# Optimization experiments

Hardware: AMD Instinct MI355X
Metric: run time of the kernel (lower is better)

The kernel has to match this reference:

```python
import jax, jax.numpy as jnp
import numpy as np

N_NODES = 100000


def gcn_conv(x, src, dst, W, b, n_nodes):
    """PyG GCNConv: out = D^{-1/2} (A + I) D^{-1/2} (x @ W) + b.
    src/dst are the original (non-self-loop) edges; self loops handled analytically.
    """
    h = x @ W  # [N, out]
    ones = jnp.ones(src.shape[0], dtype=h.dtype)
    # degree including self loop
    deg = jax.ops.segment_sum(ones, dst, num_segments=n_nodes) + 1.0  # [N]
    dinv = jax.lax.rsqrt(deg)
    norm = dinv[src] * dinv[dst]  # [E]
    msg = h[src] * norm[:, None]  # gather + scale
    agg = jax.ops.segment_sum(msg, dst, num_segments=n_nodes)  # scatter-add
    # self-loop contribution: norm = deg^{-1/2} * deg^{-1/2} = 1/deg
    agg = agg + h * (1.0 / deg)[:, None]
    return agg + b


def setup_inputs() -> dict:
    key = jax.random.key(0)
    k1, k2, k3, k4 = jax.random.split(key, 4)
    n, e = N_NODES, 3200000
    x = jax.random.normal(k1, (n, 256), dtype=jnp.float32)
    edge_index = jax.random.randint(k2, (2, e), 0, n, dtype=jnp.int64)
    W1 = jax.random.normal(k3, (256, 64), dtype=jnp.float32) * (1.0 / np.sqrt(256))
    b1 = jnp.zeros((64,), dtype=jnp.float32)
    W2 = jax.random.normal(k4, (64, 4), dtype=jnp.float32) * (1.0 / np.sqrt(64))
    b2 = jnp.zeros((4,), dtype=jnp.float32)
    return {"x": x, "edge_index": edge_index, "W1": W1, "b1": b1, "W2": W2, "b2": b2}


def reference(x, edge_index, W1, b1, W2, b2):
    n = x.shape[0]
    src, dst = edge_index[0], edge_index[1]
    h = gcn_conv(x, src, dst, W1, b1, n)
    h = jax.nn.leaky_relu(h, negative_slope=0.01)  # nn.LeakyReLU default
    # F.dropout in eval mode is identity
    h = gcn_conv(h, src, dst, W2, b2, n)
    return jax.nn.softmax(h, axis=1)
```

## Files before the change

### kernel.cpp

```cpp
#include <hip/hip_runtime.h>
#include <hip/hip_bf16.h>
#include <math.h>


#define NB 256
#define MAXB 512
#define SCHUNK 12544

typedef __attribute__((ext_vector_type(8))) short bf16x8;
typedef __attribute__((ext_vector_type(4))) float f32x4;
typedef __attribute__((ext_vector_type(2))) float f32x2;
typedef __attribute__((ext_vector_type(4))) float nf4;

__device__ __forceinline__ int edge_val(const void* ep, size_t idx, int is64) {
    if (is64) return (int)(((const long long*)ep)[idx]);
    return ((const int*)ep)[idx];
}

__device__ __forceinline__ int detect64(const unsigned int* __restrict__ ew, int E) {
    const int lane = (int)(threadIdx.x & 63);
    const int idx = (lane < E) ? (2 * lane + 1) : 1;
    const unsigned long long m = __ballot(ew[idx] != 0u);
    return m == 0ull ? 1 : 0;
}

__device__ __forceinline__ unsigned short f2bf(float f) {
    unsigned int u = __float_as_uint(f);
    return (unsigned short)((u + 0x7FFFu + ((u >> 16) & 1u)) >> 16);
}

__device__ __forceinline__ void acc_fp8row(unsigned int r, float& a0, float& a1,
                                           float& a2, float& a3) {
    const f32x2 lo = __builtin_amdgcn_cvt_pk_f32_fp8((int)r, false);
    const f32x2 hi = __builtin_amdgcn_cvt_pk_f32_fp8((int)r, true);
    a0 += lo[0]; a1 += lo[1]; a2 += hi[0]; a3 += hi[1];
}

__device__ __forceinline__ unsigned char f32_to_fp8(float f) {
    const int enc = __builtin_amdgcn_cvt_pk_fp8_f32(f, 0.f, 0, false);
    return (unsigned char)(enc & 0xff);
}

__global__ __launch_bounds__(256) void hist_pass(
    const void* __restrict__ edges, int E, int* __restrict__ ghist, int B) {
    __shared__ int hist[MAXB];
    const int tid = threadIdx.x;
    for (int i = tid; i < B; i += 256) hist[i] = 0;
    const int is64 = detect64((const unsigned int*)edges, E);
    __syncthreads();
    const int per = (E + NB - 1) / NB;
    const int s0 = blockIdx.x * per;
    const int s1 = min(s0 + per, E);
    for (int i = s0 + tid; i < s1; i += 256) {
        const int d = edge_val(edges, (size_t)E + i, is64);
        atomicAdd(&hist[d >> 8], 1);
    }
    __syncthreads();
    for (int i = tid; i < B; i += 256) ghist[(size_t)blockIdx.x * B + i] = hist[i];
}

__global__ __launch_bounds__(NB) void col_scan(
    const int* __restrict__ ghist, int* __restrict__ goff,
    int* __restrict__ bsum, int B) {
    __shared__ int sm[NB];
    const int tid = threadIdx.x;
    const int b = blockIdx.x;
    const int v = ghist[(size_t)tid * B + b];
    sm[tid] = v;
    __syncthreads();
    for (int off = 1; off < NB; off <<= 1) {
        int val = (tid >= off) ? sm[tid - off] : 0;
        __syncthreads();
        sm[tid] += val;
        __syncthreads();
    }
    goff[(size_t)tid * B + b] = sm[tid] - v;
    if (tid == NB - 1) bsum[b] = sm[tid];
}

__global__ __launch_bounds__(512) void base_scan(
    const int* __restrict__ bsum, int* __restrict__ bbase,
    int* __restrict__ row_ptr, int B, int n, int E) {
    __shared__ int sm[512];
    const int tid = threadIdx.x;
    const int v = (tid < B) ? bsum[tid] : 0;
    sm[tid] = v;
    __syncthreads();
    for (int off = 1; off < 512; off <<= 1) {
        int val = (tid >= off) ? sm[tid - off] : 0;
        __syncthreads();
        sm[tid] += val;
        __syncthreads();
    }
    if (tid < B) bbase[tid] = sm[tid] - v;
    if (tid == 0) { bbase[B] = E; row_ptr[n] = E; }
}

__global__ __launch_bounds__(512) void scatter_pass(
    const void* __restrict__ edges, int E,
    const int* __restrict__ ghist, const int* __restrict__ goff,
    const int* __restrict__ bbase, unsigned int* __restrict__ ebuf, int B) {
    __shared__ unsigned int buf[SCHUNK];
    __shared__ int lb[MAXB];
    __shared__ int lf[MAXB];
    __shared__ int sm[MAXB];
    const int tid = threadIdx.x;
    const int blk = blockIdx.x;
    const int is64 = detect64((const unsigned int*)edges, E);
    const int per = (E + NB - 1) / NB;
    const int s0 = blk * per;
    const int s1 = min(s0 + per, E);

    if (per <= SCHUNK) {
        const int c = (tid < B) ? ghist[(size_t)blk * B + tid] : 0;
        sm[tid] = c;
        __syncthreads();
        for (int off = 1; off < MAXB; off <<= 1) {
            int val = (tid >= off) ? sm[tid - off] : 0;
            __syncthreads();
            sm[tid] += val;
            __syncthreads();
        }
        if (tid < B) { lb[tid] = sm[tid] - c; lf[tid] = sm[tid] - c; }
        __syncthreads();
        for (int i = s0 + tid; i < s1; i += 512) {
            const int d = edge_val(edges, (size_t)E + i, is64);
            const int s = edge_val(edges, (size_t)i, is64);
            const unsigned int val = ((unsigned int)s << 8) | (unsigned int)(d & 255);
            const int pos = atomicAdd(&lf[d >> 8], 1);
            buf[pos] = val;
        }
        __syncthreads();
        const int lane = tid & 63;
        const int wv = tid >> 6;
        for (int b = wv; b < B; b += 8) {
            const int lo = lb[b];
            const int cnt = lf[b] - lo;
            if (cnt > 0) {
                unsigned int* dst = ebuf + bbase[b] + goff[(size_t)blk * B + b];
                for (int k = lane; k < cnt; k += 64) dst[k] = buf[lo + k];
            }
        }
    } else {
        for (int i = tid; i < B; i += 512)
            lf[i] = bbase[i] + goff[(size_t)blk * B + i];
        __syncthreads();
        for (int i = s0 + tid; i < s1; i += 512) {
            const int d = edge_val(edges, (size_t)E + i, is64);
            const int s = edge_val(edges, (size_t)i, is64);
            const int pos = atomicAdd(&lf[d >> 8], 1);
            ebuf[pos] = ((unsigned int)s << 8) | (unsigned int)(d & 255);
        }
    }
}

__global__ __launch_bounds__(512) void bucket_csr(
    const unsigned int* __restrict__ ebuf, const int* __restrict__ bbase,
    int* __restrict__ row_ptr, float* __restrict__ dinv,
    int* __restrict__ col_src, int n) {
    __shared__ int hist[256];
    __shared__ int scn[256];
    __shared__ int fill[256];
    const int tid = threadIdx.x;
    const int b = blockIdx.x;
    if (tid < 256) hist[tid] = 0;
    __syncthreads();
    const int base = bbase[b];
    const int m = bbase[b + 1] - base;
    const unsigned int* eb = ebuf + base;
    for (int i = tid; i < m; i += 512) atomicAdd(&hist[eb[i] & 255u], 1);
    __syncthreads();
    if (tid < 256) scn[tid] = hist[tid];
    __syncthreads();
    for (int off = 1; off < 256; off <<= 1) {
        int val = 0;
        if (tid < 256 && tid >= off) val = scn[tid - off];
        __syncthreads();
        if (tid < 256) scn[tid] += val;
        __syncthreads();
    }
    if (tid < 256) {
        const int excl = scn[tid] - hist[tid];
        fill[tid] = excl;
        const int v = b * 256 + tid;
        if (v < n) {
            row_ptr[v] = base + excl;
            dinv[v] = rsqrtf((float)hist[tid] + 1.0f);
        }
    }
    __syncthreads();
    for (int i = tid; i < m; i += 512) {
        const unsigned int e = eb[i];
        const int p = atomicAdd(&fill[e & 255u], 1);
        col_src[base + p] = (int)(e >> 8);
    }
}

__global__ __launch_bounds__(256) void gemm1_kernel(
    const float* __restrict__ x, const float* __restrict__ W1,
    const float* __restrict__ dinv, unsigned char* __restrict__ hs1f8, int n) {
    __shared__ unsigned short wt[64 * 264];
    const int tid = threadIdx.x;
    for (int i = tid; i < 4096; i += 256) {
        const int k = i >> 4;
        const int c0 = (i & 15) * 4;
        const float4 w = *((const float4*)W1 + i);
        wt[(c0 + 0) * 264 + k] = f2bf(w.x);
        wt[(c0 + 1) * 264 + k] = f2bf(w.y);
        wt[(c0 + 2) * 264 + k] = f2bf(w.z);
        wt[(c0 + 3) * 264 + k] = f2bf(w.w);
    }
    __syncthreads();

    const int lane = tid & 63;
    const int wid = tid >> 6;
    const int row0 = blockIdx.x * 64 + wid * 16;
    const int rr = lane & 15;
    const int kh = lane >> 4;

    union FragU { bf16x8 v; unsigned short u[8]; };
    bf16x8 af[8];
    {
        int r = row0 + rr;
        if (r >= n) r = n - 1;
        const float* xr = x + (size_t)r * 256 + kh * 8;
#pragma unroll
        for (int ks = 0; ks < 8; ++ks) {
            const nf4 p0 = __builtin_nontemporal_load((const nf4*)(xr + ks * 32));
            const nf4 p1 = __builtin_nontemporal_load((const nf4*)(xr + ks * 32 + 4));
            FragU f;
            f.u[0] = f2bf(p0[0]); f.u[1] = f2bf(p0[1]);
            f.u[2] = f2bf(p0[2]); f.u[3] = f2bf(p0[3]);
            f.u[4] = f2bf(p1[0]); f.u[5] = f2bf(p1[1]);
            f.u[6] = f2bf(p1[2]); f.u[7] = f2bf(p1[3]);
            af[ks] = f.v;
        }
    }
    f32x4 acc[4];
#pragma unroll
    for (int ct = 0; ct < 4; ++ct) acc[ct] = (f32x4){0.f, 0.f, 0.f, 0.f};
#pragma unroll
    for (int ct = 0; ct < 4; ++ct) {
        const unsigned short* wcol = wt + (ct * 16 + rr) * 264 + kh * 8;
#pragma unroll
        for (int ks = 0; ks < 8; ++ks) {
            const bf16x8 bf = *(const bf16x8*)(wcol + ks * 32);
            acc[ct] = __builtin_amdgcn_mfma_f32_16x16x32_bf16(af[ks], bf, acc[ct], 0, 0, 0);
        }
    }
#pragma unroll
    for (int j = 0; j < 4; ++j) {
        const int gr = row0 + kh * 4 + j;
        if (gr < n) {
            const float dv = dinv[gr];
#pragma unroll
            for (int ct = 0; ct < 4; ++ct)
                hs1f8[(size_t)gr * 64 + ct * 16 + rr] = f32_to_fp8(acc[ct][j] * dv);
        }
    }
}

__global__ __launch_bounds__(256) void agg1_kernel(
    const int* __restrict__ row_ptr, const int* __restrict__ col_src,
    const unsigned char* __restrict__ hs1f8, const float* __restrict__ dinv,
    const float* __restrict__ b1, const float* __restrict__ W2,
    float* __restrict__ hs2, int n) {
    const int tid = threadIdx.x;
    const int q = tid & 15;
    const int v = blockIdx.x * 16 + (tid >> 4);
    if (v >= n) return;
    const int rs = row_ptr[v];
    const int re = row_ptr[v + 1];
    float a0 = 0.f, a1 = 0.f, a2 = 0.f, a3 = 0.f;
    int e = rs;
    for (; e + 16 <= re; e += 16) {
        const int cs = col_src[e + q];
        unsigned int r[16];
#pragma unroll
        for (int j = 0; j < 16; ++j) {
            const int s = __shfl(cs, j, 16);
            r[j] = *(const unsigned int*)(hs1f8 + (size_t)s * 64 + q * 4);
        }
#pragma unroll
        for (int j = 0; j < 16; ++j) acc_fp8row(r[j], a0, a1, a2, a3);
    }
    const int rem = re - e;
    if (rem > 0) {
        const int cs = col_src[(q < rem) ? e + q : re - 1];
        for (int j = 0; j < rem; ++j) {
            const int s = __shfl(cs, j, 16);
            const unsigned int r = *(const unsigned int*)(hs1f8 + (size_t)s * 64 + q * 4);
            acc_fp8row(r, a0, a1, a2, a3);
        }
    }
    float s0 = 0.f, s1 = 0.f, s2 = 0.f, s3 = 0.f;
    acc_fp8row(*(const unsigned int*)(hs1f8 + (size_t)v * 64 + q * 4), s0, s1, s2, s3);
    const float dv = dinv[v];
    const float4 bb = ((const float4*)b1)[q];
    float4 res;
    res.x = dv * (a0 + s0) + bb.x;
    res.y = dv * (a1 + s1) + bb.y;
    res.z = dv * (a2 + s2) + bb.z;
    res.w = dv * (a3 + s3) + bb.w;
    res.x = res.x > 0.f ? res.x : 0.01f * res.x;
    res.y = res.y > 0.f ? res.y : 0.01f * res.y;
    res.z = res.z > 0.f ? res.z : 0.01f * res.z;
    res.w = res.w > 0.f ? res.w : 0.01f * res.w;
    const float4* W2v = (const float4*)W2;
    const float4 w0 = W2v[q * 4 + 0], w1 = W2v[q * 4 + 1];
    const float4 w2 = W2v[q * 4 + 2], w3 = W2v[q * 4 + 3];
    float4 p;
    p.x = res.x * w0.x + res.y * w1.x + res.z * w2.x + res.w * w3.x;
    p.y = res.x * w0.y + res.y * w1.y + res.z * w2.y + res.w * w3.y;
    p.z = res.x * w0.z + res.y * w1.z + res.z * w2.z + res.w * w3.z;
    p.w = res.x * w0.w + res.y * w1.w + res.z * w2.w + res.w * w3.w;
#pragma unroll
    for (int s = 1; s < 16; s <<= 1) {
        p.x += __shfl_xor(p.x, s, 16); p.y += __shfl_xor(p.y, s, 16);
        p.z += __shfl_xor(p.z, s, 16); p.w += __shfl_xor(p.w, s, 16);
    }
    if (q == 0) {
        float4 o; o.x = p.x * dv; o.y = p.y * dv; o.z = p.z * dv; o.w = p.w * dv;
        *(float4*)(hs2 + (size_t)v * 4) = o;
    }
}

__global__ __launch_bounds__(256) void agg2_kernel(
    const int* __restrict__ row_ptr, const int* __restrict__ col_src,
    const float* __restrict__ hs2, const float* __restrict__ dinv,
    const float* __restrict__ b2, float* __restrict__ out, int n) {
    const int lane = threadIdx.x & 63;
    int v = blockIdx.x * 4 + (threadIdx.x >> 6);
    v = __builtin_amdgcn_readfirstlane(v);
    if (v >= n) return;
    const int c = lane & 3;
    const int ei = lane >> 2;
    const int rs = row_ptr[v];
    const int re = row_ptr[v + 1];
    float acc = 0.f;
    for (int e0 = rs; e0 < re; e0 += 16) {
        const int e = e0 + ei;
        if (e < re) {
            const int s = col_src[e];
            acc += hs2[(size_t)s * 4 + c];
        }
    }
    acc += __shfl_xor(acc, 4);
    acc += __shfl_xor(acc, 8);
    acc += __shfl_xor(acc, 16);
    acc += __shfl_xor(acc, 32);
    const float val = dinv[v] * (acc + hs2[(size_t)v * 4 + c]) + b2[c];
    float m = fmaxf(val, __shfl_xor(val, 1));
    m = fmaxf(m, __shfl_xor(m, 2));
    const float ex = __expf(val - m);
    float s = ex + __shfl_xor(ex, 1);
    s += __shfl_xor(s, 2);
    if (lane < 4) out[(size_t)v * 4 + c] = ex / s;
}

extern "C" void kernel_launch(void* const* d_in, const int* in_sizes, int n_in,
                              void* d_out, int out_size, void* d_ws, size_t ws_size,
                              hipStream_t stream) {
    const float* x  = (const float*)d_in[0];
    const void*  ei = d_in[1];
    const float* W1 = (const float*)d_in[2];
    const float* b1 = (const float*)d_in[3];
    const float* W2 = (const float*)d_in[4];
    const float* b2 = (const float*)d_in[5];
    const int n = in_sizes[0] / 256;
    const int E = in_sizes[1] / 2;
    const int B = (n + 255) / 256;

    char* ws = (char*)d_ws;
    size_t off = 0;
    auto alloc = [&](size_t bytes) -> void* {
        void* p = ws + off;
        off += (bytes + 255) & ~(size_t)255;
        return p;
    };
    int*   ghist   = (int*)alloc(sizeof(int) * (size_t)NB * B);
    int*   goff    = (int*)alloc(sizeof(int) * (size_t)NB * B);
    int*   bsum    = (int*)alloc(sizeof(int) * B);
    int*   bbase   = (int*)alloc(sizeof(int) * (B + 1));
    int*   row_ptr = (int*)alloc(sizeof(int) * (n + 1));
    int*   col_src = (int*)alloc(sizeof(int) * (size_t)E);
    float* dinv    = (float*)alloc(sizeof(float) * n);
    unsigned char* hs1f8 = (unsigned char*)alloc(sizeof(unsigned char) * (size_t)n * 64);
    float* hs2     = (float*)alloc(sizeof(float) * (size_t)n * 4);
    unsigned int* ebuf = (unsigned int*)alloc(sizeof(unsigned int) * (size_t)E);
    (void)n_in; (void)out_size; (void)ws_size;

    hist_pass<<<NB, 256, 0, stream>>>(ei, E, ghist, B);
    col_scan<<<B, NB, 0, stream>>>(ghist, goff, bsum, B);
    base_scan<<<1, 512, 0, stream>>>(bsum, bbase, row_ptr, B, n, E);
    scatter_pass<<<NB, 512, 0, stream>>>(ei, E, ghist, goff, bbase, ebuf, B);
    bucket_csr<<<B, 512, 0, stream>>>(ebuf, bbase, row_ptr, dinv, col_src, n);
    gemm1_kernel<<<(n + 63) / 64, 256, 0, stream>>>(x, W1, dinv, hs1f8, n);
    agg1_kernel<<<(n + 15) / 16, 256, 0, stream>>>(row_ptr, col_src, hs1f8, dinv, b1, W2, hs2, n);
    agg2_kernel<<<(n + 3) / 4, 256, 0, stream>>>(row_ptr, col_src, hs2, dinv, b2, (float*)d_out, n);
}
```

Baseline: 189.4 us.

## Fuse CSR build passes into one cooperative kernel with grid syncs

Replaces the five separate CSR-construction launches (histogram, column scan, base scan, scatter, bucket sort) with a single cooperative kernel of 256 blocks that separates the phases with grid-wide barriers. The aim is to remove per-launch overhead and inter-kernel gaps. The trade-off is fewer blocks in the col_scan and bucket phases (256 blocks looping over B buckets instead of B blocks) and 512-thread blocks limited to one block per CU. The old kernels stay as a fallback if the cooperative launch fails.

```diff
diff --git a/kernel.cpp b/kernel.cpp
--- a/kernel.cpp
+++ b/kernel.cpp
@@ -1,6 +1,9 @@
 #include <hip/hip_runtime.h>
 #include <hip/hip_bf16.h>
+#include <hip/hip_cooperative_groups.h>
 #include <math.h>
+
+namespace cg = cooperative_groups;
 
 
 #define NB 256
@@ -39,6 +42,147 @@
 __device__ __forceinline__ unsigned char f32_to_fp8(float f) {
     const int enc = __builtin_amdgcn_cvt_pk_fp8_f32(f, 0.f, 0, false);
     return (unsigned char)(enc & 0xff);
+}
+
+__global__ __launch_bounds__(512, 1) void build_kernel(
+    const void* __restrict__ edges, int E, int* __restrict__ ghist,
+    int* __restrict__ goff, int* __restrict__ bsum, int* __restrict__ bbase,
+    int* __restrict__ row_ptr, float* __restrict__ dinv,
+    int* __restrict__ col_src, unsigned int* __restrict__ ebuf, int n, int B) {
+    cg::grid_group grid = cg::this_grid();
+    __shared__ unsigned int buf[SCHUNK];
+    __shared__ int sm[MAXB];
+    __shared__ int lb[MAXB];
+    __shared__ int lf[MAXB];
+    const int tid = threadIdx.x;
+    const int blk = blockIdx.x;
+    const int is64 = detect64((const unsigned int*)edges, E);
+    const int per = (E + NB - 1) / NB;
+    const int s0 = blk * per;
+    const int s1 = min(s0 + per, E);
+
+    for (int i = tid; i < B; i += 512) lf[i] = 0;
+    __syncthreads();
+    for (int i = s0 + tid; i < s1; i += 512) {
+        const int d = edge_val(edges, (size_t)E + i, is64);
+        atomicAdd(&lf[d >> 8], 1);
+    }
+    __syncthreads();
+    for (int i = tid; i < B; i += 512) ghist[(size_t)blk * B + i] = lf[i];
+    grid.sync();
+
+    {
+        const int col = blk + ((tid >> 8) << 8);
+        const int t = tid & 255;
+        const bool act = col < B;
+        const int v = act ? ghist[(size_t)t * B + col] : 0;
+        sm[tid] = v;
+        __syncthreads();
+        for (int off = 1; off < 256; off <<= 1) {
+            const int val = (t >= off) ? sm[tid - off] : 0;
+            __syncthreads();
+            sm[tid] += val;
+            __syncthreads();
+        }
+        if (act) {
+            goff[(size_t)t * B + col] = sm[tid] - v;
+            if (t == 255) bsum[col] = sm[tid];
+        }
+    }
+    grid.sync();
+
+    if (blk == 0) {
+        const int v = (tid < B) ? bsum[tid] : 0;
+        sm[tid] = v;
+        __syncthreads();
+        for (int off = 1; off < 512; off <<= 1) {
+            const int val = (tid >= off) ? sm[tid - off] : 0;
+            __syncthreads();
+            sm[tid] += val;
+            __syncthreads();
+        }
+        if (tid < B) bbase[tid] = sm[tid] - v;
+        if (tid == 0) { bbase[B] = E; row_ptr[n] = E; }
+    }
+    grid.sync();
+
+    if (per <= SCHUNK) {
+        const int c = (tid < B) ? ghist[(size_t)blk * B + tid] : 0;
+        sm[tid] = c;
+        __syncthreads();
+        for (int off = 1; off < MAXB; off <<= 1) {
+            const int val = (tid >= off) ? sm[tid - off] : 0;
+            __syncthreads();
+            sm[tid] += val;
+            __syncthreads();
+        }
+        if (tid < B) { lb[tid] = sm[tid] - c; lf[tid] = sm[tid] - c; }
+        __syncthreads();
+        for (int i = s0 + tid; i < s1; i += 512) {
+            const int d = edge_val(edges, (size_t)E + i, is64);
+            const int s = edge_val(edges, (size_t)i, is64);
+            const unsigned int val = ((unsigned int)s << 8) | (unsigned int)(d & 255);
+            const int pos = atomicAdd(&lf[d >> 8], 1);
+            buf[pos] = val;
+        }
+        __syncthreads();
+        const int lane = tid & 63;
+        const int wv = tid >> 6;
+        for (int b = wv; b < B; b += 8) {
+            const int lo = lb[b];
+            const int cnt = lf[b] - lo;
+            if (cnt > 0) {
+                unsigned int* dst = ebuf + bbase[b] + goff[(size_t)blk * B + b];
+                for (int k = lane; k < cnt; k += 64) dst[k] = buf[lo + k];
+            }
+        }
+    } else {
+        for (int i = tid; i < B; i += 512)
+            lf[i] = bbase[i] + goff[(size_t)blk * B + i];
+        __syncthreads();
+        for (int i = s0 + tid; i < s1; i += 512) {
+            const int d = edge_val(edges, (size_t)E + i, is64);
+            const int s = edge_val(edges, (size_t)i, is64);
+            const int pos = atomicAdd(&lf[d >> 8], 1);
+            ebuf[pos] = ((unsigned int)s << 8) | (unsigned int)(d & 255);
+        }
+    }
+    grid.sync();
+
+    for (int bb = blk; bb < B; bb += NB) {
+        __syncthreads();
+        if (tid < 256) sm[tid] = 0;
+        __syncthreads();
+        const int base = bbase[bb];
+        const int m = bbase[bb + 1] - base;
+        const unsigned int* eb = ebuf + base;
+        for (int i = tid; i < m; i += 512) atomicAdd(&sm[eb[i] & 255u], 1);
+        __syncthreads();
+        if (tid < 256) lb[tid] = sm[tid];
+        __syncthreads();
+        for (int off = 1; off < 256; off <<= 1) {
+            int val = 0;
+            if (tid < 256 && tid >= off) val = lb[tid - off];
+            __syncthreads();
+            if (tid < 256) lb[tid] += val;
+            __syncthreads();
+        }
+        if (tid < 256) {
+            const int excl = lb[tid] - sm[tid];
+            lf[tid] = excl;
+            const int v = bb * 256 + tid;
+            if (v < n) {
+                row_ptr[v] = base + excl;
+                dinv[v] = rsqrtf((float)sm[tid] + 1.0f);
+            }
+        }
+        __syncthreads();
+        for (int i = tid; i < m; i += 512) {
+            const unsigned int e = eb[i];
+            const int p = atomicAdd(&lf[e & 255u], 1);
+            col_src[base + p] = (int)(e >> 8);
+        }
+    }
 }
 
 __global__ __launch_bounds__(256) void hist_pass(
@@ -110,7 +254,6 @@
     const int per = (E + NB - 1) / NB;
     const int s0 = blk * per;
     const int s1 = min(s0 + per, E);
-
     if (per <= SCHUNK) {
         const int c = (tid < B) ? ghist[(size_t)blk * B + tid] : 0;
         sm[tid] = c;
@@ -367,9 +510,9 @@
     const float* b1 = (const float*)d_in[3];
     const float* W2 = (const float*)d_in[4];
     const float* b2 = (const float*)d_in[5];
-    const int n = in_sizes[0] / 256;
-    const int E = in_sizes[1] / 2;
-    const int B = (n + 255) / 256;
+    int n = in_sizes[0] / 256;
+    int E = in_sizes[1] / 2;
+    int B = (n + 255) / 256;
 
     char* ws = (char*)d_ws;
     size_t off = 0;
@@ -390,11 +533,19 @@
     unsigned int* ebuf = (unsigned int*)alloc(sizeof(unsigned int) * (size_t)E);
     (void)n_in; (void)out_size; (void)ws_size;
 
-    hist_pass<<<NB, 256, 0, stream>>>(ei, E, ghist, B);
-    col_scan<<<B, NB, 0, stream>>>(ghist, goff, bsum, B);
-    base_scan<<<1, 512, 0, stream>>>(bsum, bbase, row_ptr, B, n, E);
-    scatter_pass<<<NB, 512, 0, stream>>>(ei, E, ghist, goff, bbase, ebuf, B);
-    bucket_csr<<<B, 512, 0, stream>>>(ebuf, bbase, row_ptr, dinv, col_src, n);
+    void* args[] = {(void*)&ei, (void*)&E, (void*)&ghist, (void*)&goff,
+                    (void*)&bsum, (void*)&bbase, (void*)&row_ptr, (void*)&dinv,
+                    (void*)&col_src, (void*)&ebuf, (void*)&n, (void*)&B};
+    hipError_t cerr = hipLaunchCooperativeKernel((void*)build_kernel, dim3(NB),
+                                                 dim3(512), args, 0, stream);
+    if (cerr != hipSuccess) {
+        (void)hipGetLastError();
+        hist_pass<<<NB, 256, 0, stream>>>(ei, E, ghist, B);
+        col_scan<<<B, NB, 0, stream>>>(ghist, goff, bsum, B);
+        base_scan<<<1, 512, 0, stream>>>(bsum, bbase, row_ptr, B, n, E);
+        scatter_pass<<<NB, 512, 0, stream>>>(ei, E, ghist, goff, bbase, ebuf, B);
+        bucket_csr<<<B, 512, 0, stream>>>(ebuf, bbase, row_ptr, dinv, col_src, n);
+    }
     gemm1_kernel<<<(n + 63) / 64, 256, 0, stream>>>(x, W1, dinv, hs1f8, n);
     agg1_kernel<<<(n + 15) / 16, 256, 0, stream>>>(row_ptr, col_src, hs1f8, dinv, b1, W2, hs2, n);
     agg2_kernel<<<(n + 3) / 4, 256, 0, stream>>>(row_ptr, col_src, hs2, dinv, b2, (float*)d_out, n);
```

Result: slower. 310.9 us (+64.1%).
